# Kernel optimization log

Hardware: AMD Instinct MI355X
Metric: run time of the kernel (lower is better)

The kernel has to match this reference:

```python
import jax, jax.numpy as jnp
import numpy as np

N, C, H, W_DIM = 32, 256, 64, 64


def setup_inputs() -> dict:
    key = jax.random.key(0)
    ks = jax.random.split(key, 7)
    x = jax.random.normal(ks[0], (N, C, H, W_DIM), dtype=jnp.float32)
    # 1x1 conv weights stored as 2-D matrices (out_ch, in_ch)
    W2 = jax.random.normal(ks[1], (C, C), dtype=jnp.float32) / np.sqrt(C).astype(np.float32)
    W8 = jax.random.normal(ks[2], (C, 25), dtype=jnp.float32) / np.sqrt(25.0).astype(np.float32)
    W10 = jax.random.normal(ks[3], (H * 25, C), dtype=jnp.float32) / np.sqrt(C).astype(np.float32)
    W18 = jax.random.normal(ks[4], (C * H,), dtype=jnp.float32)
    p4 = 0.02 * jax.random.normal(ks[5], (1, 1, H, W_DIM), dtype=jnp.float32)
    p13 = 0.02 * jax.random.normal(ks[6], (1, H, W_DIM), dtype=jnp.float32)
    return {"x": x, "W2": W2, "W8": W8, "W10": W10, "W18": W18, "p4": p4, "p13": p13}


def reference(x, W2, W8, W10, W18, p4, p13):
    n = x.shape[0]
    t1 = jax.nn.relu(x)                                  # (n,c,h,w)
    t2 = jnp.einsum('oc,nchw->nohw', W2, t1)             # 1x1 conv p_2
    t3 = t1.max(axis=(2, 3))                             # global max -> (n,c)
    t5 = (p4 * t2).mean(axis=1)                          # (n,h,w)
    # F.unfold(kernel=(5,5), dilation=3, padding=6): size-preserving dilated patches
    pad5 = jnp.pad(t5, ((0, 0), (6, 6), (6, 6)))
    t6 = jnp.stack(
        [pad5[:, 3 * ki:3 * ki + H, 3 * kj:3 * kj + W_DIM]
         for ki in range(5) for kj in range(5)],
        axis=1)                                          # (n,25,h,w), (ki,kj) row-major like torch
    t7 = t6.max(axis=2)                                  # max over h -> (n,25,w)
    t8 = jnp.einsum('ok,nkw->now', W8, t7)               # 1x1 conv p_8 -> (n,c,w)
    t9 = jnp.einsum('nc,nchw->nhw', t3, x)               # bmm global context -> (n,h,w)
    t10 = jnp.einsum('oc,ncw->now', W10, t8)             # 1x1 conv p_10 -> (n,25h,w)
    t11 = jax.nn.gelu(t10, approximate=False)            # torch F.gelu default = exact erf
    t12 = t6.reshape(n, 25 * H, W_DIM) + t11             # (n,25h,w)
    t13 = p13 * t9                                       # (n,h,w)
    t14 = jnp.exp(t12)
    # F.unfold(kernel=(1,7), dilation=(1,3), padding=(0,9)) along w, size-preserving
    padw = jnp.pad(t14, ((0, 0), (0, 0), (9, 9)))
    t15 = jnp.stack([padw[:, :, 3 * j:3 * j + W_DIM] for j in range(7)], axis=2)  # (n,25h,7,w)
    t16 = t15.max(axis=1)                                # (n,7,w)
    t17 = t16.mean(axis=1)                               # (n,w)
    t18 = W18[None, :, None] * t17[:, None, :]           # 1x1 conv p_18 (in_ch=1) -> (n,c*h,w)
    t19 = t13[:, None, :, :] - t18.reshape(n, C, H, W_DIM)
    return t19
```

## Files before the change

### kernel.cpp

```cpp
#include <hip/hip_runtime.h>
#include <math.h>

#define NB 32
#define C 256
#define H 64
#define W 64
#define HW 4096
#define KT 25

__global__ __launch_bounds__(256) void k0_ww(
    const float* __restrict__ W10, const float* __restrict__ W8,
    float* __restrict__ WW) {
  __shared__ float s8[256 * 25];
  int tid = threadIdx.x;
  for (int i = tid; i < 6400; i += 256) s8[i] = W8[i];
  __syncthreads();
  int idx = blockIdx.x * 256 + tid;
  if (idx >= 1600 * 25) return;
  int o = idx / 25, kk = idx - o * 25;
  const float* wrow = W10 + (size_t)o * 256;
  float acc = 0.f;
#pragma unroll 8
  for (int c = 0; c < 256; ++c) acc = fmaf(wrow[c], s8[c * 25 + kk], acc);
  WW[idx] = acc;
}

__global__ __launch_bounds__(256) void k1_t3_prep(
    const float* __restrict__ x, const float* __restrict__ W2,
    float* __restrict__ w2bar, float* __restrict__ t3) {
  int b = blockIdx.x;
  int tid = threadIdx.x;
  if (b == NB * C) {
    float s = 0.f;
    for (int o = 0; o < C; ++o) s += W2[o * C + tid];
    w2bar[tid] = s * (1.0f / (float)C);
    return;
  }
  const float4* xv = (const float4*)(x + (size_t)b * HW);
  float m = -3.4e38f;
#pragma unroll
  for (int i = 0; i < 4; ++i) {
    float4 v = xv[i * 256 + tid];
    m = fmaxf(m, fmaxf(fmaxf(v.x, v.y), fmaxf(v.z, v.w)));
  }
  for (int off = 32; off > 0; off >>= 1)
    m = fmaxf(m, __shfl_down(m, off, 64));
  __shared__ float sm[4];
  if ((tid & 63) == 0) sm[tid >> 6] = m;
  __syncthreads();
  if (tid == 0) {
    float mm = fmaxf(fmaxf(sm[0], sm[1]), fmaxf(sm[2], sm[3]));
    t3[b] = fmaxf(mm, 0.0f);
  }
}

__global__ __launch_bounds__(256) void k2_s_t9(
    const float* __restrict__ x, const float* __restrict__ w2bar,
    const float* __restrict__ t3, const float* __restrict__ p4,
    const float* __restrict__ p13, float* __restrict__ t5,
    float* __restrict__ t13) {
  int n = blockIdx.x >> 4;
  int p = ((blockIdx.x & 15) << 8) | threadIdx.x;
  __shared__ float sw[C];
  __shared__ float st[C];
  sw[threadIdx.x] = w2bar[threadIdx.x];
  st[threadIdx.x] = t3[n * C + threadIdx.x];
  __syncthreads();
  const float* xp = x + (size_t)n * C * HW + p;
  float accs = 0.f, acc9 = 0.f;
#pragma unroll 16
  for (int c = 0; c < C; ++c) {
    float v = xp[(size_t)c * HW];
    accs = fmaf(sw[c], fmaxf(v, 0.f), accs);
    acc9 = fmaf(st[c], v, acc9);
  }
  t5[n * HW + p] = p4[p] * accs;
  t13[n * HW + p] = p13[p] * acc9;
}

__global__ __launch_bounds__(256) void k4_fused(
    const float* __restrict__ t5g, const float* __restrict__ WW,
    float* __restrict__ part) {
  int n = blockIdx.x / KT;
  int k = blockIdx.x - n * KT;
  int ki = k / 5, kj = k - ki * 5;
  int tid = threadIdx.x;
  int wg = tid & 15, w0 = wg * 4;
  int rg = tid >> 4, h0 = rg * 4;
  __shared__ float s5[HW];
  __shared__ float ww[64 * 25];
  __shared__ float t7s[25 * 64];
  __shared__ float cm[5 * 64];

  const float4* t5v = (const float4*)(t5g + n * HW);
  float4* s5v = (float4*)s5;
#pragma unroll
  for (int i = 0; i < 4; ++i) s5v[i * 256 + tid] = t5v[i * 256 + tid];
  const float* wwsrc = WW + (size_t)k * 64 * 25;
  for (int i = tid; i < 1600; i += 256) ww[i] = wwsrc[i];
  __syncthreads();

  for (int idx = tid; idx < 5 * 64; idx += 256) {
    int kii = idx >> 6, wp = idx & 63;
    int lo = max(0, 3 * kii - 6), hi = min(63, 3 * kii + 57);
    float m = (kii == 2) ? -3.4e38f : 0.0f;
    for (int hp = lo; hp <= hi; ++hp) m = fmaxf(m, s5[hp * 64 + wp]);
    cm[kii * 64 + wp] = m;
  }
  __syncthreads();
  for (int idx = tid; idx < 25 * 64; idx += 256) {
    int kk = idx >> 6, w = idx & 63;
    int kki = kk / 5, kkj = kk - kki * 5;
    int wp = w + 3 * kkj - 6;
    t7s[kk * 64 + w] = (wp >= 0 && wp < 64) ? cm[kki * 64 + wp] : 0.0f;
  }
  __syncthreads();

  float4 acc[4];
#pragma unroll
  for (int j = 0; j < 4; ++j) acc[j] = make_float4(0.f, 0.f, 0.f, 0.f);
#pragma unroll
  for (int kk = 0; kk < 25; ++kk) {
    float4 tv = *(const float4*)&t7s[kk * 64 + w0];
#pragma unroll
    for (int j = 0; j < 4; ++j) {
      float a = ww[(h0 + j) * 25 + kk];
      acc[j].x = fmaf(a, tv.x, acc[j].x);
      acc[j].y = fmaf(a, tv.y, acc[j].y);
      acc[j].z = fmaf(a, tv.z, acc[j].z);
      acc[j].w = fmaf(a, tv.w, acc[j].w);
    }
  }

  int hpb = 3 * ki - 6, wpb = 3 * kj - 6;
  float pm[4] = {-3.4e38f, -3.4e38f, -3.4e38f, -3.4e38f};
#pragma unroll
  for (int j = 0; j < 4; ++j) {
    int hp = h0 + j + hpb;
    float av[4] = {acc[j].x, acc[j].y, acc[j].z, acc[j].w};
#pragma unroll
    for (int e = 0; e < 4; ++e) {
      int wp = w0 + e + wpb;
      float t6v = (hp >= 0 && hp < 64 && wp >= 0 && wp < 64)
                      ? s5[hp * 64 + wp] : 0.0f;
      float xg = av[e];
      float gl = 0.5f * xg * (1.0f + erff(xg * 0.70710678118654752f));
      pm[e] = fmaxf(pm[e], t6v + gl);
    }
  }
  __syncthreads();
  float* red = t7s;
#pragma unroll
  for (int e = 0; e < 4; ++e) red[rg * 64 + w0 + e] = pm[e];
  __syncthreads();
  if (tid < 64) {
    float m = -3.4e38f;
#pragma unroll
    for (int g = 0; g < 16; ++g) m = fmaxf(m, red[g * 64 + tid]);
    part[(n * KT + k) * 64 + tid] = m;
  }
}

__global__ __launch_bounds__(64) void k5_t17(
    const float* __restrict__ part, float* __restrict__ t17) {
  int n = blockIdx.x;
  int w = threadIdx.x;
  float m = -3.4e38f;
#pragma unroll
  for (int t = 0; t < KT; ++t)
    m = fmaxf(m, part[(n * KT + t) * 64 + w]);
  __shared__ float M[64];
  M[w] = expf(m);
  __syncthreads();
  float s = 0.f;
#pragma unroll
  for (int j = 0; j < 7; ++j) {
    int wp = w + 3 * j - 9;
    if (wp >= 0 && wp < 64) s += M[wp];
  }
  t17[n * 64 + w] = s * (1.0f / 7.0f);
}

__global__ __launch_bounds__(256) void k6_out(
    const float* __restrict__ t13, const float* __restrict__ t17,
    const float* __restrict__ W18, float* __restrict__ out) {
  int b = blockIdx.x;
  int n = b >> 8, c = b & 255;
  int tid = threadIdx.x;
  const float4* t13v = (const float4*)(t13 + n * HW);
  const float4* t17v = (const float4*)(t17 + n * 64);
  float4* outv = (float4*)(out + (size_t)b * HW);
#pragma unroll
  for (int i = 0; i < 4; ++i) {
    int idx = i * 256 + tid;
    int h = idx >> 4;
    int w4 = idx & 15;
    float w18 = W18[c * 64 + h];
    float4 a = t13v[idx];
    float4 tt = t17v[w4];
    float4 o;
    o.x = a.x - w18 * tt.x;
    o.y = a.y - w18 * tt.y;
    o.z = a.z - w18 * tt.z;
    o.w = a.w - w18 * tt.w;
    outv[idx] = o;
  }
}

extern "C" void kernel_launch(void* const* d_in, const int* in_sizes, int n_in,
                              void* d_out, int out_size, void* d_ws,
                              size_t ws_size, hipStream_t stream) {
  const float* x   = (const float*)d_in[0];
  const float* W2  = (const float*)d_in[1];
  const float* W8  = (const float*)d_in[2];
  const float* W10 = (const float*)d_in[3];
  const float* W18 = (const float*)d_in[4];
  const float* p4  = (const float*)d_in[5];
  const float* p13 = (const float*)d_in[6];
  float* out = (float*)d_out;

  float* ws    = (float*)d_ws;
  float* w2bar = ws;
  float* t3    = w2bar + 256;
  float* t5    = t3 + NB * C;
  float* t13   = t5 + NB * HW;
  float* WW    = t13 + NB * HW;
  float* part  = WW + 1600 * 25;
  float* t17   = part + NB * KT * 64;

  k0_ww<<<dim3(157), dim3(256), 0, stream>>>(W10, W8, WW);
  k1_t3_prep<<<dim3(NB * C + 1), dim3(256), 0, stream>>>(x, W2, w2bar, t3);
  k2_s_t9<<<dim3(NB * 16), dim3(256), 0, stream>>>(x, w2bar, t3, p4, p13, t5, t13);
  k4_fused<<<dim3(NB * KT), dim3(256), 0, stream>>>(t5, WW, part);
  k5_t17<<<dim3(NB), dim3(64), 0, stream>>>(part, t17);
  k6_out<<<dim3(NB * C), dim3(256), 0, stream>>>(t13, t17, W18, out);
}
```

Baseline: 311.3 us.

## Merge prep kernels, split channel reduction, and fold t17 into output kernel

Combines the WW precompute, w2bar and per-channel max into one launch, with each wave handling one (n,c) max so fewer blocks are needed. The t5/t13 channel reduction now splits channels across two thread halves and doubles the block count to raise parallelism. The t17 computation is folded into the output kernel, which stages t13 in shared memory and writes 8 channels per block. This cuts two launches and the separate t17 pass, at the cost of recomputing t17 redundantly in each output block.

```diff
diff --git a/kernel.cpp b/kernel.cpp
--- a/kernel.cpp
+++ b/kernel.cpp
@@ -8,77 +8,86 @@
 #define HW 4096
 #define KT 25
 
-__global__ __launch_bounds__(256) void k0_ww(
-    const float* __restrict__ W10, const float* __restrict__ W8,
+__global__ __launch_bounds__(256) void ka_prep(
+    const float* __restrict__ x, const float* __restrict__ W2,
+    const float* __restrict__ W8, const float* __restrict__ W10,
+    float* __restrict__ w2bar, float* __restrict__ t3,
     float* __restrict__ WW) {
-  __shared__ float s8[256 * 25];
-  int tid = threadIdx.x;
-  for (int i = tid; i < 6400; i += 256) s8[i] = W8[i];
-  __syncthreads();
-  int idx = blockIdx.x * 256 + tid;
-  if (idx >= 1600 * 25) return;
-  int o = idx / 25, kk = idx - o * 25;
-  const float* wrow = W10 + (size_t)o * 256;
-  float acc = 0.f;
+  int bid = blockIdx.x, tid = threadIdx.x;
+  if (bid < 157) {
+    __shared__ float s8[6400];
+    for (int i = tid; i < 6400; i += 256) s8[i] = W8[i];
+    __syncthreads();
+    int idx = bid * 256 + tid;
+    if (idx < 40000) {
+      int o = idx / 25, kk = idx - o * 25;
+      const float* wrow = W10 + (size_t)o * 256;
+      float acc = 0.f;
 #pragma unroll 8
-  for (int c = 0; c < 256; ++c) acc = fmaf(wrow[c], s8[c * 25 + kk], acc);
-  WW[idx] = acc;
-}
-
-__global__ __launch_bounds__(256) void k1_t3_prep(
-    const float* __restrict__ x, const float* __restrict__ W2,
-    float* __restrict__ w2bar, float* __restrict__ t3) {
-  int b = blockIdx.x;
-  int tid = threadIdx.x;
-  if (b == NB * C) {
+      for (int c = 0; c < 256; ++c) acc = fmaf(wrow[c], s8[c * 25 + kk], acc);
+      WW[idx] = acc;
+    }
+  } else if (bid == 157) {
     float s = 0.f;
-    for (int o = 0; o < C; ++o) s += W2[o * C + tid];
-    w2bar[tid] = s * (1.0f / (float)C);
-    return;
-  }
-  const float4* xv = (const float4*)(x + (size_t)b * HW);
-  float m = -3.4e38f;
-#pragma unroll
-  for (int i = 0; i < 4; ++i) {
-    float4 v = xv[i * 256 + tid];
-    m = fmaxf(m, fmaxf(fmaxf(v.x, v.y), fmaxf(v.z, v.w)));
-  }
-  for (int off = 32; off > 0; off >>= 1)
-    m = fmaxf(m, __shfl_down(m, off, 64));
-  __shared__ float sm[4];
-  if ((tid & 63) == 0) sm[tid >> 6] = m;
-  __syncthreads();
-  if (tid == 0) {
-    float mm = fmaxf(fmaxf(sm[0], sm[1]), fmaxf(sm[2], sm[3]));
-    t3[b] = fmaxf(mm, 0.0f);
-  }
-}
-
-__global__ __launch_bounds__(256) void k2_s_t9(
+#pragma unroll 8
+    for (int o = 0; o < 256; ++o) s += W2[o * 256 + tid];
+    w2bar[tid] = s * (1.f / 256.f);
+  } else {
+    int item = (bid - 158) * 4 + (tid >> 6);
+    int lane = tid & 63;
+    const float4* xv = (const float4*)(x + (size_t)item * HW);
+    float m = -3.4e38f;
+#pragma unroll
+    for (int i = 0; i < 16; ++i) {
+      float4 v = xv[i * 64 + lane];
+      m = fmaxf(m, fmaxf(fmaxf(v.x, v.y), fmaxf(v.z, v.w)));
+    }
+#pragma unroll
+    for (int off = 32; off > 0; off >>= 1)
+      m = fmaxf(m, __shfl_down(m, off, 64));
+    if (lane == 0) t3[item] = fmaxf(m, 0.f);
+  }
+}
+
+__global__ __launch_bounds__(256) void kb_t5t13(
     const float* __restrict__ x, const float* __restrict__ w2bar,
     const float* __restrict__ t3, const float* __restrict__ p4,
     const float* __restrict__ p13, float* __restrict__ t5,
     float* __restrict__ t13) {
-  int n = blockIdx.x >> 4;
-  int p = ((blockIdx.x & 15) << 8) | threadIdx.x;
-  __shared__ float sw[C];
-  __shared__ float st[C];
-  sw[threadIdx.x] = w2bar[threadIdx.x];
-  st[threadIdx.x] = t3[n * C + threadIdx.x];
-  __syncthreads();
-  const float* xp = x + (size_t)n * C * HW + p;
+  int bid = blockIdx.x, tid = threadIdx.x;
+  int n = bid >> 5;
+  int pc = bid & 31;
+  int half = tid >> 7;
+  int lp = tid & 127;
+  int p = pc * 128 + lp;
+  __shared__ float sw[256];
+  __shared__ float st[256];
+  __shared__ float r5[256];
+  __shared__ float r9[256];
+  sw[tid] = w2bar[tid];
+  st[tid] = t3[n * 256 + tid];
+  __syncthreads();
+  const float* xp = x + (size_t)n * C * HW + (size_t)half * 128 * HW + p;
   float accs = 0.f, acc9 = 0.f;
 #pragma unroll 16
-  for (int c = 0; c < C; ++c) {
+  for (int c = 0; c < 128; ++c) {
     float v = xp[(size_t)c * HW];
-    accs = fmaf(sw[c], fmaxf(v, 0.f), accs);
-    acc9 = fmaf(st[c], v, acc9);
-  }
-  t5[n * HW + p] = p4[p] * accs;
-  t13[n * HW + p] = p13[p] * acc9;
-}
-
-__global__ __launch_bounds__(256) void k4_fused(
+    accs = fmaf(sw[half * 128 + c], fmaxf(v, 0.f), accs);
+    acc9 = fmaf(st[half * 128 + c], v, acc9);
+  }
+  r5[tid] = accs;
+  r9[tid] = acc9;
+  __syncthreads();
+  if (tid < 128) {
+    int pp = pc * 128 + tid;
+    float as = r5[tid] + r5[tid + 128];
+    float a9 = r9[tid] + r9[tid + 128];
+    t5[n * HW + pp] = p4[pp] * as;
+    t13[n * HW + pp] = p13[pp] * a9;
+  }
+}
+
+__global__ __launch_bounds__(256) void kc_tile(
     const float* __restrict__ t5g, const float* __restrict__ WW,
     float* __restrict__ part) {
   int n = blockIdx.x / KT;
@@ -161,49 +170,59 @@
   }
 }
 
-__global__ __launch_bounds__(64) void k5_t17(
-    const float* __restrict__ part, float* __restrict__ t17) {
-  int n = blockIdx.x;
-  int w = threadIdx.x;
-  float m = -3.4e38f;
-#pragma unroll
-  for (int t = 0; t < KT; ++t)
-    m = fmaxf(m, part[(n * KT + t) * 64 + w]);
-  __shared__ float M[64];
-  M[w] = expf(m);
-  __syncthreads();
-  float s = 0.f;
-#pragma unroll
-  for (int j = 0; j < 7; ++j) {
-    int wp = w + 3 * j - 9;
-    if (wp >= 0 && wp < 64) s += M[wp];
-  }
-  t17[n * 64 + w] = s * (1.0f / 7.0f);
-}
-
-__global__ __launch_bounds__(256) void k6_out(
-    const float* __restrict__ t13, const float* __restrict__ t17,
+__global__ __launch_bounds__(256) void kd_out(
+    const float* __restrict__ part, const float* __restrict__ t13,
     const float* __restrict__ W18, float* __restrict__ out) {
-  int b = blockIdx.x;
-  int n = b >> 8, c = b & 255;
-  int tid = threadIdx.x;
-  const float4* t13v = (const float4*)(t13 + n * HW);
-  const float4* t17v = (const float4*)(t17 + n * 64);
-  float4* outv = (float4*)(out + (size_t)b * HW);
-#pragma unroll
-  for (int i = 0; i < 4; ++i) {
-    int idx = i * 256 + tid;
-    int h = idx >> 4;
-    int w4 = idx & 15;
-    float w18 = W18[c * 64 + h];
-    float4 a = t13v[idx];
-    float4 tt = t17v[w4];
-    float4 o;
-    o.x = a.x - w18 * tt.x;
-    o.y = a.y - w18 * tt.y;
-    o.z = a.z - w18 * tt.z;
-    o.w = a.w - w18 * tt.w;
-    outv[idx] = o;
+  int bid = blockIdx.x, tid = threadIdx.x;
+  int n = bid >> 5, cg8 = bid & 31;
+  __shared__ float ps[1600];
+  __shared__ float Mb[64];
+  __shared__ float t17b[64];
+  __shared__ float t13s[4096];
+  const float* pp = part + (size_t)n * KT * 64;
+  for (int i = tid; i < 1600; i += 256) ps[i] = pp[i];
+  const float4* t13v = (const float4*)(t13 + (size_t)n * HW);
+  float4* t13sv = (float4*)t13s;
+#pragma unroll
+  for (int i = 0; i < 4; ++i) t13sv[i * 256 + tid] = t13v[i * 256 + tid];
+  __syncthreads();
+  if (tid < 64) {
+    float m = -3.4e38f;
+#pragma unroll
+    for (int t = 0; t < KT; ++t) m = fmaxf(m, ps[t * 64 + tid]);
+    Mb[tid] = expf(m);
+  }
+  __syncthreads();
+  if (tid < 64) {
+    float s = 0.f;
+#pragma unroll
+    for (int j = 0; j < 7; ++j) {
+      int wp = tid + 3 * j - 9;
+      if (wp >= 0 && wp < 64) s += Mb[wp];
+    }
+    t17b[tid] = s * (1.0f / 7.0f);
+  }
+  __syncthreads();
+  const float4* t17v = (const float4*)t17b;
+#pragma unroll
+  for (int i = 0; i < 8; ++i) {
+    int c = cg8 * 8 + i;
+    float4* outv = (float4*)(out + (size_t)(n * 256 + c) * HW);
+#pragma unroll
+    for (int it = 0; it < 4; ++it) {
+      int idx = it * 256 + tid;
+      int h = idx >> 4;
+      int w4 = idx & 15;
+      float w18 = W18[c * 64 + h];
+      float4 a = t13sv[idx];
+      float4 tt = t17v[w4];
+      float4 o;
+      o.x = a.x - w18 * tt.x;
+      o.y = a.y - w18 * tt.y;
+      o.z = a.z - w18 * tt.z;
+      o.w = a.w - w18 * tt.w;
+      outv[idx] = o;
+    }
   }
 }
 
@@ -225,13 +244,12 @@
   float* t5    = t3 + NB * C;
   float* t13   = t5 + NB * HW;
   float* WW    = t13 + NB * HW;
-  float* part  = WW + 1600 * 25;
-  float* t17   = part + NB * KT * 64;
-
-  k0_ww<<<dim3(157), dim3(256), 0, stream>>>(W10, W8, WW);
-  k1_t3_prep<<<dim3(NB * C + 1), dim3(256), 0, stream>>>(x, W2, w2bar, t3);
-  k2_s_t9<<<dim3(NB * 16), dim3(256), 0, stream>>>(x, w2bar, t3, p4, p13, t5, t13);
-  k4_fused<<<dim3(NB * KT), dim3(256), 0, stream>>>(t5, WW, part);
-  k5_t17<<<dim3(NB), dim3(64), 0, stream>>>(part, t17);
-  k6_out<<<dim3(NB * C), dim3(256), 0, stream>>>(t13, t17, W18, out);
-}
+  float* part  = WW + 40000;
+
+  ka_prep<<<dim3(158 + 2048), dim3(256), 0, stream>>>(x, W2, W8, W10, w2bar,
+                                                      t3, WW);
+  kb_t5t13<<<dim3(NB * 32), dim3(256), 0, stream>>>(x, w2bar, t3, p4, p13,
+                                                    t5, t13);
+  kc_tile<<<dim3(NB * KT), dim3(256), 0, stream>>>(t5, WW, part);
+  kd_out<<<dim3(NB * 32), dim3(256), 0, stream>>>(part, t13, W18, out);
+}
```

After: 299.4 us. -3.8%, faster.
